# Kernel tuning notes

Measured on AMD Instinct MI355X. Metric: run time of the kernel, lower is better.

## Reference

```python
import jax, jax.numpy as jnp
import numpy as np

BATCH = 4096
TEMP = 0.5
WORLD = 1
B = BATCH * WORLD
N = 2 * B
DIM = 128


def _neg_indices():
    # mask_correlated_samples: ones(N,N) with diagonal and the two +/-B
    # off-diagonals zeroed; negatives are entries where mask is True.
    mask = np.ones((N, N), dtype=bool)
    np.fill_diagonal(mask, False)
    idx = np.arange(B)
    mask[idx, idx + B] = False
    mask[idx + B, idx] = False
    rows, cols = np.nonzero(mask)  # each row has exactly N-2 negatives
    return rows.reshape(N, N - 2), cols.reshape(N, N - 2)

_NEG_ROWS, _NEG_COLS = _neg_indices()


def setup_inputs() -> dict:
    key = jax.random.key(0)
    k1, k2 = jax.random.split(key)
    z_i = jax.random.normal(k1, (BATCH, DIM), dtype=jnp.float32)
    z_j = jax.random.normal(k2, (BATCH, DIM), dtype=jnp.float32)
    return {"z_i": z_i, "z_j": z_j}


def reference(z_i, z_j):
    z = jnp.concatenate([z_i, z_j], axis=0)                 # [N, D]
    z = z / jnp.linalg.norm(z, axis=1, keepdims=True)       # L2 normalize
    # cosine similarity of unit vectors == dot product
    sim = (z @ z.T) / TEMP                                   # [N, N]
    sim_i_j = jnp.diagonal(sim, offset=B)                    # [B]
    sim_j_i = jnp.diagonal(sim, offset=-B)                   # [B]
    pos = jnp.concatenate([sim_i_j, sim_j_i])[:, None]       # [N, 1]
    neg = sim[_NEG_ROWS, _NEG_COLS]                          # [N, N-2]
    logits = jnp.concatenate([pos, neg], axis=1)             # [N, N-1]
    # CrossEntropyLoss(reduction='sum') with labels all zero, then / N
    loss = jnp.sum(jax.scipy.special.logsumexp(logits, axis=1) - logits[:, 0])
    return loss / N
```

## Files before the change

### kernel.cpp

```cpp
#include <hip/hip_runtime.h>
#include <hip/hip_bf16.h>


#define NN 8192
#define BHALF 4096
#define DIMK 128

typedef __bf16 bf16x8 __attribute__((ext_vector_type(8)));
typedef float f32x4 __attribute__((ext_vector_type(4)));

#define C1F 2.8853900817779268f
#define SCALEF 1.6986436f

__global__ __launch_bounds__(256) void nt_normalize(
    const float* __restrict__ zi, const float* __restrict__ zj,
    unsigned int* __restrict__ zb_packed, float* __restrict__ out) {
  if (blockIdx.x == 0 && threadIdx.x == 0) out[0] = 0.0f;
  int row = blockIdx.x * 4 + (threadIdx.x >> 6);
  int lane = threadIdx.x & 63;
  const float* src = (row < BHALF) ? (zi + (size_t)row * DIMK)
                                   : (zj + (size_t)(row - BHALF) * DIMK);
  float2 v = ((const float2*)src)[lane];
  float ss = v.x * v.x + v.y * v.y;
#pragma unroll
  for (int off = 32; off >= 1; off >>= 1) ss += __shfl_xor(ss, off, 64);
  float rn = rsqrtf(ss) * SCALEF;
  __hip_bfloat16 h0 = __float2bfloat16(v.x * rn);
  __hip_bfloat16 h1 = __float2bfloat16(v.y * rn);
  unsigned int packed = ((unsigned int)(*(unsigned short*)&h1) << 16) |
                        (*(unsigned short*)&h0);
  int tile = row >> 4, t = row & 15;
  int cq = lane >> 2;
  int c = cq >> 2, quad = cq & 3;
  size_t widx = ((size_t)((tile * 4 + c) * 64 + quad * 16 + t)) * 4 + (lane & 3);
  zb_packed[widx] = packed;
}

__global__ __launch_bounds__(256, 2) void nt_sim(
    const uint4* __restrict__ zbv, float* __restrict__ part) {
  __shared__ uint4 ldsb[4096];

  const int lane = threadIdx.x & 63;
  const int wave = threadIdx.x >> 6;
  const int quad = lane >> 4;
  const int t = lane & 15;
  const int row_tile0 = blockIdx.y * 16 + wave * 4;

  {
    const char* gsrc = (const char*)zbv + (size_t)blockIdx.x * 65536;
#pragma unroll
    for (int k = 0; k < 16; ++k) {
      int chunk = k * 4 + wave;
      __builtin_amdgcn_global_load_lds(
          (const __attribute__((address_space(1))) unsigned int*)(
              gsrc + chunk * 1024 + lane * 16),
          (__attribute__((address_space(3))) unsigned int*)(
              (char*)ldsb + chunk * 1024),
          16, 0, 0);
    }
  }

  bf16x8 A[4][4];
#pragma unroll
  for (int rt = 0; rt < 4; ++rt)
#pragma unroll
    for (int c = 0; c < 4; ++c)
      A[rt][c] = __builtin_bit_cast(
          bf16x8, zbv[(size_t)((row_tile0 + rt) * 4 + c) * 64 + lane]);

  float sum[4][4];
#pragma unroll
  for (int rt = 0; rt < 4; ++rt)
#pragma unroll
    for (int r = 0; r < 4; ++r) sum[rt][r] = 0.f;

  __syncthreads();

#pragma unroll 2
  for (int ct = 0; ct < 16; ++ct) {
    f32x4 acc[4];
#pragma unroll
    for (int rt = 0; rt < 4; ++rt) acc[rt] = (f32x4){0.f, 0.f, 0.f, 0.f};
#pragma unroll
    for (int c = 0; c < 4; ++c) {
      bf16x8 bv = __builtin_bit_cast(bf16x8, ldsb[(ct * 4 + c) * 64 + lane]);
#pragma unroll
      for (int rt = 0; rt < 4; ++rt)
        acc[rt] = __builtin_amdgcn_mfma_f32_16x16x32_bf16(A[rt][c], bv,
                                                          acc[rt], 0, 0, 0);
    }
#pragma unroll
    for (int rt = 0; rt < 4; ++rt)
#pragma unroll
      for (int r = 0; r < 4; ++r)
        sum[rt][r] += __builtin_amdgcn_exp2f(acc[rt][r]);
  }

#pragma unroll
  for (int off = 8; off >= 1; off >>= 1)
#pragma unroll
    for (int rt = 0; rt < 4; ++rt)
#pragma unroll
      for (int r = 0; r < 4; ++r)
        sum[rt][r] += __shfl_xor(sum[rt][r], off, 16);

  if (t == 0) {
    float* dst = part + (size_t)blockIdx.x * NN;
    int row_base = row_tile0 * 16;
#pragma unroll
    for (int rt = 0; rt < 4; ++rt)
#pragma unroll
      for (int r = 0; r < 4; ++r)
        dst[row_base + rt * 16 + quad * 4 + r] = sum[rt][r];
  }
}

__device__ __forceinline__ float bf2f(unsigned short s) {
  unsigned int u = (unsigned int)s << 16;
  return __builtin_bit_cast(float, u);
}

__global__ __launch_bounds__(256) void nt_finalize(
    const uint4* __restrict__ zbv, const float* __restrict__ part,
    float* __restrict__ out) {
  int i = blockIdx.x * 256 + threadIdx.x;
  int tile = i >> 4, t = i & 15;
  int p = i ^ BHALF;
  int tilep = p >> 4;
  float S = 0.f;
#pragma unroll
  for (int k = 0; k < 32; ++k) S += part[(size_t)k * NN + i];
  float dp = 0.f, dd = 0.f;
#pragma unroll
  for (int cq = 0; cq < 16; ++cq) {
    int c = cq >> 2, q = cq & 3;
    uint4 ua = zbv[(size_t)((tile * 4 + c) * 64 + q * 16 + t)];
    uint4 up = zbv[(size_t)((tilep * 4 + c) * 64 + q * 16 + t)];
    const unsigned short* pa = (const unsigned short*)&ua;
    const unsigned short* pp = (const unsigned short*)&up;
#pragma unroll
    for (int k = 0; k < 8; ++k) {
      float a = bf2f(pa[k]), pv = bf2f(pp[k]);
      dd = fmaf(a, a, dd);
      dp = fmaf(a, pv, dp);
    }
  }
  float diag = __builtin_amdgcn_exp2f(dd);
  float v = logf(S - diag) - (2.0f / C1F) * dp;
#pragma unroll
  for (int off = 32; off >= 1; off >>= 1) v += __shfl_xor(v, off, 64);
  __shared__ float wsum[4];
  if ((threadIdx.x & 63) == 0) wsum[threadIdx.x >> 6] = v;
  __syncthreads();
  if (threadIdx.x == 0)
    atomicAdd(out, (wsum[0] + wsum[1] + wsum[2] + wsum[3]) * (1.0f / (float)NN));
}

extern "C" void kernel_launch(void* const* d_in, const int* in_sizes, int n_in,
                              void* d_out, int out_size, void* d_ws,
                              size_t ws_size, hipStream_t stream) {
  const float* zi = (const float*)d_in[0];
  const float* zj = (const float*)d_in[1];

  unsigned int* zb = (unsigned int*)d_ws;
  float* part = (float*)((char*)d_ws + (2u << 20));

  nt_normalize<<<NN / 4, 256, 0, stream>>>(zi, zj, zb, (float*)d_out);

  dim3 grid(32, 32);
  nt_sim<<<grid, 256, 0, stream>>>((const uint4*)zb, part);

  nt_finalize<<<NN / 256, 256, 0, stream>>>((const uint4*)zb, part,
                                            (float*)d_out);
}
```

Before: 79.57 us.

## Exploit similarity matrix symmetry to compute only upper-triangle tiles

Splits the 8192x8192 similarity into 64x64 blocks of 128 rows and computes only the diagonal and upper-triangle blocks, mapping a linear block id to (bi,bj) with a sqrt-based triangular index. Each off-diagonal block writes both row sums and column sums (via a small LDS buffer) so the transpose block is never computed. This roughly halves the MFMA and exp2 work. In exchange it adds column reductions, extra shared memory traffic and smaller 128-thread blocks, and the finalize kernel now reduces 64 partials instead of 32.

After: 82.34 us. +3.5%, slower.

```diff
diff --git a/kernel.cpp b/kernel.cpp
--- a/kernel.cpp
+++ b/kernel.cpp
@@ -36,82 +36,116 @@
   zb_packed[widx] = packed;
 }
 
-__global__ __launch_bounds__(256, 2) void nt_sim(
+__global__ __launch_bounds__(128, 2) void nt_sim(
     const uint4* __restrict__ zbv, float* __restrict__ part) {
-  __shared__ uint4 ldsb[4096];
+  __shared__ uint4 ldsb[2048];
+  __shared__ float colbuf[2][128];
 
   const int lane = threadIdx.x & 63;
   const int wave = threadIdx.x >> 6;
   const int quad = lane >> 4;
   const int t = lane & 15;
-  const int row_tile0 = blockIdx.y * 16 + wave * 4;
-
-  {
-    const char* gsrc = (const char*)zbv + (size_t)blockIdx.x * 65536;
-#pragma unroll
-    for (int k = 0; k < 16; ++k) {
-      int chunk = k * 4 + wave;
-      __builtin_amdgcn_global_load_lds(
-          (const __attribute__((address_space(1))) unsigned int*)(
-              gsrc + chunk * 1024 + lane * 16),
-          (__attribute__((address_space(3))) unsigned int*)(
-              (char*)ldsb + chunk * 1024),
-          16, 0, 0);
-    }
+
+  const int u = blockIdx.x;
+  const bool offdiag = (u >= 32);
+  int bi, bj;
+  if (!offdiag) {
+    bi = u; bj = u;
+  } else {
+    int v = u - 32;
+    bi = (int)((127.0f - sqrtf(16129.0f - 8.0f * (float)v)) * 0.5f);
+    while ((bi + 1) * (127 - (bi + 1)) / 2 <= v) ++bi;
+    while (bi * (127 - bi) / 2 > v) --bi;
+    bj = bi + 1 + (v - bi * (127 - bi) / 2);
   }
-
-  bf16x8 A[4][4];
-#pragma unroll
-  for (int rt = 0; rt < 4; ++rt)
-#pragma unroll
-    for (int c = 0; c < 4; ++c)
-      A[rt][c] = __builtin_bit_cast(
-          bf16x8, zbv[(size_t)((row_tile0 + rt) * 4 + c) * 64 + lane]);
-
-  float sum[4][4];
-#pragma unroll
-  for (int rt = 0; rt < 4; ++rt)
-#pragma unroll
-    for (int r = 0; r < 4; ++r) sum[rt][r] = 0.f;
-
-  __syncthreads();
+  const int npass = offdiag ? 1 : 2;
+
+  for (int pass = 0; pass < npass; ++pass) {
+    if (pass) {
+      bi += 32; bj += 32;
+      __syncthreads();
+    }
+
+    {
+      const char* gsrc = (const char*)zbv + (size_t)bj * 32768;
+#pragma unroll
+      for (int k = 0; k < 16; ++k) {
+        int chunk = k * 2 + wave;
+        __builtin_amdgcn_global_load_lds(
+            (const __attribute__((address_space(1))) unsigned int*)(
+                gsrc + chunk * 1024 + lane * 16),
+            (__attribute__((address_space(3))) unsigned int*)(
+                (char*)ldsb + chunk * 1024),
+            16, 0, 0);
+      }
+    }
+
+    const int row_tile0 = bi * 8 + wave * 4;
+    bf16x8 A[4][4];
+#pragma unroll
+    for (int rt = 0; rt < 4; ++rt)
+#pragma unroll
+      for (int c = 0; c < 4; ++c)
+        A[rt][c] = __builtin_bit_cast(
+            bf16x8, zbv[(size_t)((row_tile0 + rt) * 4 + c) * 64 + lane]);
+
+    float sum[4][4];
+#pragma unroll
+    for (int rt = 0; rt < 4; ++rt)
+#pragma unroll
+      for (int r = 0; r < 4; ++r) sum[rt][r] = 0.f;
+
+    __syncthreads();
 
 #pragma unroll 2
-  for (int ct = 0; ct < 16; ++ct) {
-    f32x4 acc[4];
-#pragma unroll
-    for (int rt = 0; rt < 4; ++rt) acc[rt] = (f32x4){0.f, 0.f, 0.f, 0.f};
-#pragma unroll
-    for (int c = 0; c < 4; ++c) {
-      bf16x8 bv = __builtin_bit_cast(bf16x8, ldsb[(ct * 4 + c) * 64 + lane]);
+    for (int ct = 0; ct < 8; ++ct) {
+      f32x4 acc[4];
+#pragma unroll
+      for (int rt = 0; rt < 4; ++rt) acc[rt] = (f32x4){0.f, 0.f, 0.f, 0.f};
+#pragma unroll
+      for (int c = 0; c < 4; ++c) {
+        bf16x8 bv = __builtin_bit_cast(bf16x8, ldsb[(ct * 4 + c) * 64 + lane]);
+#pragma unroll
+        for (int rt = 0; rt < 4; ++rt)
+          acc[rt] = __builtin_amdgcn_mfma_f32_16x16x32_bf16(A[rt][c], bv,
+                                                            acc[rt], 0, 0, 0);
+      }
+      float cs = 0.f;
 #pragma unroll
       for (int rt = 0; rt < 4; ++rt)
-        acc[rt] = __builtin_amdgcn_mfma_f32_16x16x32_bf16(A[rt][c], bv,
-                                                          acc[rt], 0, 0, 0);
-    }
-#pragma unroll
-    for (int rt = 0; rt < 4; ++rt)
-#pragma unroll
-      for (int r = 0; r < 4; ++r)
-        sum[rt][r] += __builtin_amdgcn_exp2f(acc[rt][r]);
-  }
-
-#pragma unroll
-  for (int off = 8; off >= 1; off >>= 1)
-#pragma unroll
-    for (int rt = 0; rt < 4; ++rt)
-#pragma unroll
-      for (int r = 0; r < 4; ++r)
-        sum[rt][r] += __shfl_xor(sum[rt][r], off, 16);
-
-  if (t == 0) {
-    float* dst = part + (size_t)blockIdx.x * NN;
-    int row_base = row_tile0 * 16;
-#pragma unroll
-    for (int rt = 0; rt < 4; ++rt)
-#pragma unroll
-      for (int r = 0; r < 4; ++r)
-        dst[row_base + rt * 16 + quad * 4 + r] = sum[rt][r];
+#pragma unroll
+        for (int r = 0; r < 4; ++r) {
+          float e = __builtin_amdgcn_exp2f(acc[rt][r]);
+          sum[rt][r] += e;
+          cs += e;
+        }
+      cs += __shfl_xor(cs, 16, 64);
+      cs += __shfl_xor(cs, 32, 64);
+      if (quad == 0) colbuf[wave][ct * 16 + t] = cs;
+    }
+
+#pragma unroll
+    for (int off = 8; off >= 1; off >>= 1)
+#pragma unroll
+      for (int rt = 0; rt < 4; ++rt)
+#pragma unroll
+        for (int r = 0; r < 4; ++r)
+          sum[rt][r] += __shfl_xor(sum[rt][r], off, 16);
+
+    if (t == 0) {
+      float* dst = part + (size_t)bj * NN + bi * 128 + wave * 64;
+#pragma unroll
+      for (int rt = 0; rt < 4; ++rt)
+#pragma unroll
+        for (int r = 0; r < 4; ++r)
+          dst[rt * 16 + quad * 4 + r] = sum[rt][r];
+    }
+
+    if (offdiag) {
+      __syncthreads();
+      part[(size_t)bi * NN + bj * 128 + threadIdx.x] =
+          colbuf[0][threadIdx.x] + colbuf[1][threadIdx.x];
+    }
   }
 }
 
@@ -129,7 +163,7 @@
   int tilep = p >> 4;
   float S = 0.f;
 #pragma unroll
-  for (int k = 0; k < 32; ++k) S += part[(size_t)k * NN + i];
+  for (int k = 0; k < 64; ++k) S += part[(size_t)k * NN + i];
   float dp = 0.f, dd = 0.f;
 #pragma unroll
   for (int cq = 0; cq < 16; ++cq) {
@@ -167,8 +201,7 @@
 
   nt_normalize<<<NN / 4, 256, 0, stream>>>(zi, zj, zb, (float*)d_out);
 
-  dim3 grid(32, 32);
-  nt_sim<<<grid, 256, 0, stream>>>((const uint4*)zb, part);
+  nt_sim<<<2048, 128, 0, stream>>>((const uint4*)zb, part);
 
   nt_finalize<<<NN / 256, 256, 0, stream>>>((const uint4*)zb, part,
                                             (float*)d_out);
```

## Fuse finalize into sim kernel via per-row-block completion counters

Applied to the files above, without the earlier changes.

Removes the separate finalize kernel launch. Each nt_sim block stores its partial row sums atomically, then increments a counter for its row block. The last of the 32 column blocks to arrive reads all partials for those rows and computes the loss contribution. This saves one launch and its tail gap, at the cost of an atomic counter per block plus serialized tail work in the last-arriving blocks.

Result: slower. 93.40 us (+17.4%).

```diff
diff --git a/kernel.cpp b/kernel.cpp
--- a/kernel.cpp
+++ b/kernel.cpp
@@ -14,8 +14,12 @@
 
 __global__ __launch_bounds__(256) void nt_normalize(
     const float* __restrict__ zi, const float* __restrict__ zj,
-    unsigned int* __restrict__ zb_packed, float* __restrict__ out) {
-  if (blockIdx.x == 0 && threadIdx.x == 0) out[0] = 0.0f;
+    unsigned int* __restrict__ zb_packed, float* __restrict__ out,
+    int* __restrict__ cnt) {
+  if (blockIdx.x == 0) {
+    if (threadIdx.x == 0) out[0] = 0.0f;
+    if (threadIdx.x < 32) cnt[threadIdx.x] = 0;
+  }
   int row = blockIdx.x * 4 + (threadIdx.x >> 6);
   int lane = threadIdx.x & 63;
   const float* src = (row < BHALF) ? (zi + (size_t)row * DIMK)
@@ -36,9 +40,17 @@
   zb_packed[widx] = packed;
 }
 
+__device__ __forceinline__ float bf2f(unsigned short s) {
+  unsigned int u = (unsigned int)s << 16;
+  return __builtin_bit_cast(float, u);
+}
+
 __global__ __launch_bounds__(256, 2) void nt_sim(
-    const uint4* __restrict__ zbv, float* __restrict__ part) {
+    const uint4* __restrict__ zbv, float* __restrict__ part,
+    int* __restrict__ cnt, float* __restrict__ out) {
   __shared__ uint4 ldsb[4096];
+  __shared__ int sdone;
+  __shared__ float wsum[4];
 
   const int lane = threadIdx.x & 63;
   const int wave = threadIdx.x >> 6;
@@ -105,55 +117,59 @@
         sum[rt][r] += __shfl_xor(sum[rt][r], off, 16);
 
   if (t == 0) {
-    float* dst = part + (size_t)blockIdx.x * NN;
-    int row_base = row_tile0 * 16;
+    float* dst = part + (size_t)blockIdx.x * NN + blockIdx.y * 256 + wave * 64;
 #pragma unroll
     for (int rt = 0; rt < 4; ++rt)
 #pragma unroll
       for (int r = 0; r < 4; ++r)
-        dst[row_base + rt * 16 + quad * 4 + r] = sum[rt][r];
+        __hip_atomic_store(&dst[rt * 16 + quad * 4 + r], sum[rt][r],
+                           __ATOMIC_RELAXED, __HIP_MEMORY_SCOPE_AGENT);
   }
-}
 
-__device__ __forceinline__ float bf2f(unsigned short s) {
-  unsigned int u = (unsigned int)s << 16;
-  return __builtin_bit_cast(float, u);
-}
+  __syncthreads();
+  if (threadIdx.x == 0) {
+    int prev = __hip_atomic_fetch_add(&cnt[blockIdx.y], 1, __ATOMIC_ACQ_REL,
+                                      __HIP_MEMORY_SCOPE_AGENT);
+    sdone = (prev == 31) ? 1 : 0;
+  }
+  __syncthreads();
+  if (!sdone) return;
 
-__global__ __launch_bounds__(256) void nt_finalize(
-    const uint4* __restrict__ zbv, const float* __restrict__ part,
-    float* __restrict__ out) {
-  int i = blockIdx.x * 256 + threadIdx.x;
-  int tile = i >> 4, t = i & 15;
-  int p = i ^ BHALF;
-  int tilep = p >> 4;
-  float S = 0.f;
+  {
+    int i = blockIdx.y * 256 + threadIdx.x;
+    int tile = i >> 4, tt = i & 15;
+    int p = i ^ BHALF;
+    int tilep = p >> 4;
+    float S = 0.f;
 #pragma unroll
-  for (int k = 0; k < 32; ++k) S += part[(size_t)k * NN + i];
-  float dp = 0.f, dd = 0.f;
+    for (int k = 0; k < 32; ++k)
+      S += __hip_atomic_load(&part[(size_t)k * NN + i], __ATOMIC_RELAXED,
+                             __HIP_MEMORY_SCOPE_AGENT);
+    float dp = 0.f, dd = 0.f;
 #pragma unroll
-  for (int cq = 0; cq < 16; ++cq) {
-    int c = cq >> 2, q = cq & 3;
-    uint4 ua = zbv[(size_t)((tile * 4 + c) * 64 + q * 16 + t)];
-    uint4 up = zbv[(size_t)((tilep * 4 + c) * 64 + q * 16 + t)];
-    const unsigned short* pa = (const unsigned short*)&ua;
-    const unsigned short* pp = (const unsigned short*)&up;
+    for (int cq = 0; cq < 16; ++cq) {
+      int c = cq >> 2, q = cq & 3;
+      uint4 ua = zbv[(size_t)((tile * 4 + c) * 64 + q * 16 + tt)];
+      uint4 up = zbv[(size_t)((tilep * 4 + c) * 64 + q * 16 + tt)];
+      const unsigned short* pa = (const unsigned short*)&ua;
+      const unsigned short* pp = (const unsigned short*)&up;
 #pragma unroll
-    for (int k = 0; k < 8; ++k) {
-      float a = bf2f(pa[k]), pv = bf2f(pp[k]);
-      dd = fmaf(a, a, dd);
-      dp = fmaf(a, pv, dp);
+      for (int k = 0; k < 8; ++k) {
+        float a = bf2f(pa[k]), pv = bf2f(pp[k]);
+        dd = fmaf(a, a, dd);
+        dp = fmaf(a, pv, dp);
+      }
     }
+    float diag = __builtin_amdgcn_exp2f(dd);
+    float v = logf(S - diag) - (2.0f / C1F) * dp;
+#pragma unroll
+    for (int off = 32; off >= 1; off >>= 1) v += __shfl_xor(v, off, 64);
+    if ((threadIdx.x & 63) == 0) wsum[threadIdx.x >> 6] = v;
+    __syncthreads();
+    if (threadIdx.x == 0)
+      atomicAdd(out,
+                (wsum[0] + wsum[1] + wsum[2] + wsum[3]) * (1.0f / (float)NN));
   }
-  float diag = __builtin_amdgcn_exp2f(dd);
-  float v = logf(S - diag) - (2.0f / C1F) * dp;
-#pragma unroll
-  for (int off = 32; off >= 1; off >>= 1) v += __shfl_xor(v, off, 64);
-  __shared__ float wsum[4];
-  if ((threadIdx.x & 63) == 0) wsum[threadIdx.x >> 6] = v;
-  __syncthreads();
-  if (threadIdx.x == 0)
-    atomicAdd(out, (wsum[0] + wsum[1] + wsum[2] + wsum[3]) * (1.0f / (float)NN));
 }
 
 extern "C" void kernel_launch(void* const* d_in, const int* in_sizes, int n_in,
@@ -164,12 +180,11 @@
 
   unsigned int* zb = (unsigned int*)d_ws;
   float* part = (float*)((char*)d_ws + (2u << 20));
+  int* cnt = (int*)((char*)d_ws + (3u << 20));
 
-  nt_normalize<<<NN / 4, 256, 0, stream>>>(zi, zj, zb, (float*)d_out);
+  nt_normalize<<<NN / 4, 256, 0, stream>>>(zi, zj, zb, (float*)d_out, cnt);
 
   dim3 grid(32, 32);
-  nt_sim<<<grid, 256, 0, stream>>>((const uint4*)zb, part);
-
-  nt_finalize<<<NN / 256, 256, 0, stream>>>((const uint4*)zb, part,
-                                            (float*)d_out);
+  nt_sim<<<grid, 256, 0, stream>>>((const uint4*)zb, part, cnt,
+                                   (float*)d_out);
 }
```
